# Kernel optimization log

Hardware: AMD Instinct MI355X
Metric: run time of the kernel (lower is better)

The kernel has to match this reference:

```python
import jax, jax.numpy as jnp
import numpy as np

L, S, R, NUM_RESNET = 6, 2, 3, 3
N = 2 ** L            # 64 blocks per axis
NX = N * S            # 128 grid points per axis
NCART_SIDE = 80
NCART = NCART_SIDE ** 2


def _perm_idx(L_, l):
    delta = 2 ** (L_ - l - 1)
    t = np.tile(np.arange(2) * delta, delta) + np.repeat(np.arange(delta), 2)
    t = np.tile(t, 2 ** l) + np.repeat(np.arange(2 ** l) * 2 ** (L_ - l), 2 ** (L_ - l))
    return jnp.asarray(t)


def _switch_idx(L_):
    h = L_ // 2
    t = np.tile(np.arange(2 ** h) * 2 ** h, 2 ** h) + np.repeat(np.arange(2 ** h), 2 ** h)
    return jnp.asarray(t)


def _bmm2(x, g_left, g_right):
    # x: (B,p,i,q,j). Right block-diag GEMM on (q,j), then left block-diag GEMM on (p,i).
    y = jnp.einsum('bpiqj,qjk->bpiqk', x, g_right)
    return jnp.einsum('bpiqk,pio->bpoqk', y, g_left)


def _complex_layer(xr, xi, p):
    # p: stacked (r1,i1,r2,i2,r3,i3,r4,i4); complex-style cross products of the original.
    r1, i1, r2, i2, r3, i3, r4, i4 = p
    yr = _bmm2(xr, r1, r1) + _bmm2(xr, i1, i1) + _bmm2(xi, r2, i2) + _bmm2(xi, i2, r2)
    yi = _bmm2(xi, r3, r3) + _bmm2(xi, i3, i3) + _bmm2(xr, r4, i4) + _bmm2(xr, i4, r4)
    return yr, yi


def _u_layer(xr, xi, p):
    ur1, ui1, ur2, ui2, ur3, ui3, ur4, ui4 = p
    return (_bmm2(xr, ur1, ur1) + _bmm2(xr, ui2, ui2)
            + _bmm2(xi, ur3, ui3) + _bmm2(xi, ui4, ur4))


def _permute(yr, yi, idx):
    yr = jnp.take(jnp.take(yr, idx, axis=1), idx, axis=3)
    yi = jnp.take(jnp.take(yi, idx, axis=1), idx, axis=3)
    return yr, yi


def _merge(y):  # (B,N,R,N,R) -> (B,N/2,2R,N/2,2R)
    return y.reshape(y.shape[0], N // 2, 2 * R, N // 2, 2 * R)


def _split(y):  # inverse of _merge
    return y.reshape(y.shape[0], N, R, N, R)


def reference(x, Vp, Hp, Mp, Gp, Up, cart_mat, r_index):
    B = x.shape[0]
    xr = x[..., 0].reshape(B, N, S, N, S)
    xi = x[..., 1].reshape(B, N, S, N, S)
    yr, yi = _complex_layer(xr, xi, Vp)                       # (B,N,R,N,R)
    for li, l in enumerate(range(L - 1, L // 2 - 1, -1)):     # H stages (permute then merge-GEMM)
        yr, yi = _permute(yr, yi, _perm_idx(L, l))
        yr, yi = _complex_layer(_merge(yr), _merge(yi), Hp[li])
        yr, yi = _split(yr), _split(yi)
    yr, yi = _permute(yr, yi, _switch_idx(L))                 # middle switch shuffle
    for k in range(NUM_RESNET):                               # residual M blocks
        zr, zi = _complex_layer(yr, yi, Mp[k])
        yr, yi = yr + zr, yi + zi
    for li, l in enumerate(range(L // 2 - 1, -1, -1)):        # G stages (merge-GEMM then permute)
        yr, yi = _complex_layer(_merge(yr), _merge(yi), Gp[li])
        yr, yi = _split(yr), _split(yi)
        yr, yi = _permute(yr, yi, _perm_idx(L, l))
    y = _u_layer(yr, yi, Up).reshape(B, NX * NX)              # real output, (B,NX,NX) flattened
    y = jnp.take(y, r_index, axis=1)                          # polar reindexing
    out = y @ cart_mat.T                                      # polar -> cartesian interpolation
    return out.reshape(B, NCART_SIDE, NCART_SIDE)


def setup_inputs() -> dict:
    key = jax.random.key(0)
    ks = jax.random.split(key, 9)
    B = 128
    x = jax.random.normal(ks[0], (B, NX, NX, 2), dtype=jnp.float32)
    Vp = jax.random.normal(ks[1], (8, N, S, R), dtype=jnp.float32) * 0.35
    Hp = jax.random.normal(ks[2], (L // 2, 8, N // 2, 2 * R, 2 * R), dtype=jnp.float32) * 0.2
    Mp = jax.random.normal(ks[3], (NUM_RESNET, 8, N, R, R), dtype=jnp.float32) * 0.25
    Gp = jax.random.normal(ks[4], (L // 2, 8, N // 2, 2 * R, 2 * R), dtype=jnp.float32) * 0.2
    Up = jax.random.normal(ks[5], (8, N, R, S), dtype=jnp.float32) * 0.35
    cart_mat = jax.random.normal(ks[6], (NCART, NX * NX), dtype=jnp.float32) * 0.01
    r_index = jax.random.permutation(ks[7], NX * NX).astype(jnp.int32)
    return {"x": x, "Vp": Vp, "Hp": Hp, "Mp": Mp, "Gp": Gp, "Up": Up,
            "cart_mat": cart_mat, "r_index": r_index}
```

## Files before the change

kernel.cpp:

```cpp
#include <hip/hip_runtime.h>


typedef __attribute__((ext_vector_type(8))) short sx8;
typedef __attribute__((ext_vector_type(4))) float fx4;
typedef __attribute__((ext_vector_type(8))) unsigned short usx8;
typedef __attribute__((ext_vector_type(4))) unsigned short usx4;

__device__ __forceinline__ unsigned short f2bf(float f) {
  unsigned u = __builtin_bit_cast(unsigned, f);
  u = (u + 0x7FFFu + ((u >> 16) & 1u)) >> 16;
  return (unsigned short)u;
}
__device__ __forceinline__ float bf2f(unsigned short h) {
  return __builtin_bit_cast(float, ((unsigned)h) << 16);
}

template<int ID>
__device__ __forceinline__ int rp_apply(int k) {
  if constexpr (ID == 0) { return k; }
  else if constexpr (ID == 3) { return (k & 7) * 8 + (k >> 3); }
  else {
    constexpr int l = (ID == 1) ? 4 : (ID == 2) ? 3 : (ID == 4) ? 2 : (ID == 5) ? 1 : 0;
    constexpr int d = 1 << (5 - l);
    constexpr int m2 = 2 * d;
    int g = k / m2, r = k % m2;
    return g * m2 + (r & 1) * d + (r >> 1);
  }
}

__global__ __launch_bounds__(256) void k_transpose(const float* __restrict__ x,
                                                   float* __restrict__ xtr,
                                                   float* __restrict__ xti) {
  __shared__ float ls[2][32][129];
  const int t = threadIdx.x;
  const int u = blockIdx.x;
  const int v0 = blockIdx.y * 32;
  for (int it = 0; it < 32; ++it) {
    int b = it * 4 + (t >> 6);
    int r = t & 63;
    int v = r >> 1, ch = r & 1;
    ls[ch][v][b] = x[(((size_t)b * 128 + u) * 128 + (v0 + v)) * 2 + ch];
  }
  __syncthreads();
  for (int it = 0; it < 32; ++it) {
    int idx = it * 256 + t;
    int ch = idx >> 12;
    int v = (idx >> 7) & 31;
    int b = idx & 127;
    float* dst = ch ? xti : xtr;
    dst[((size_t)(u * 128 + v0 + v)) * 128 + b] = ls[ch][v][b];
  }
}

__global__ __launch_bounds__(128) void k_vh(const float* __restrict__ xtr,
                                            const float* __restrict__ xti,
                                            float* __restrict__ yr,
                                            float* __restrict__ yi,
                                            const float* __restrict__ vp,
                                            const float* __restrict__ hp) {
  const int b = threadIdx.x;
  const int P = blockIdx.x, Q = blockIdx.y;
  float Vr[36], Vi[36];

#pragma unroll
  for (int pp = 0; pp < 2; ++pp)
#pragma unroll
    for (int qq = 0; qq < 2; ++qq) {
      const int p = 2 * P + pp, q = 2 * Q + qq;
      float Xr[4], Xi[4];
#pragma unroll
      for (int i = 0; i < 2; ++i)
#pragma unroll
        for (int j = 0; j < 2; ++j) {
          size_t off = ((size_t)((4 * P + 2 * pp + i) * 128 + (4 * Q + 2 * qq + j))) * 128 + b;
          Xr[i * 2 + j] = xtr[off];
          Xi[i * 2 + j] = xti[off];
        }
      float Ar[9], Ai[9];
#pragma unroll
      for (int k = 0; k < 9; ++k) { Ar[k] = 0.f; Ai[k] = 0.f; }
      auto termV = [&](float* Y, const float* X, int lm, int rm) {
        const float* Lw = vp + ((size_t)lm * 64 + p) * 6;
        const float* Rw = vp + ((size_t)rm * 64 + q) * 6;
#pragma unroll
        for (int i = 0; i < 2; ++i) {
          float t0 = X[i*2+0] * Rw[0] + X[i*2+1] * Rw[3];
          float t1 = X[i*2+0] * Rw[1] + X[i*2+1] * Rw[4];
          float t2 = X[i*2+0] * Rw[2] + X[i*2+1] * Rw[5];
#pragma unroll
          for (int o = 0; o < 3; ++o) {
            float lv = Lw[i * 3 + o];
            Y[o*3+0] += lv * t0; Y[o*3+1] += lv * t1; Y[o*3+2] += lv * t2;
          }
        }
      };
      termV(Ar, Xr, 0, 0); termV(Ar, Xr, 1, 1); termV(Ai, Xr, 6, 7); termV(Ai, Xr, 7, 6);
      termV(Ar, Xi, 2, 3); termV(Ar, Xi, 3, 2); termV(Ai, Xi, 4, 4); termV(Ai, Xi, 5, 5);
#pragma unroll
      for (int o = 0; o < 3; ++o)
#pragma unroll
        for (int k = 0; k < 3; ++k) {
          Vr[(3 * pp + o) * 6 + 3 * qq + k] = Ar[o * 3 + k];
          Vi[(3 * pp + o) * 6 + 3 * qq + k] = Ai[o * 3 + k];
        }
    }

  float Yr[36], Yi[36];
#pragma unroll
  for (int k = 0; k < 36; ++k) { Yr[k] = 0.f; Yi[k] = 0.f; }
  auto termH = [&](float* Y, const float* X, int lm, int rm) {
    const float* Lw = hp + ((size_t)lm * 32 + P) * 36;
    const float* Rw = hp + ((size_t)rm * 32 + Q) * 36;
#pragma unroll
    for (int i = 0; i < 6; ++i) {
      float tk[6];
#pragma unroll
      for (int k = 0; k < 6; ++k) tk[k] = 0.f;
#pragma unroll
      for (int j = 0; j < 6; ++j) {
        float xv = X[i * 6 + j];
#pragma unroll
        for (int k = 0; k < 6; ++k) tk[k] += xv * Rw[j * 6 + k];
      }
#pragma unroll
      for (int o = 0; o < 6; ++o) {
        float lv = Lw[i * 6 + o];
#pragma unroll
        for (int k = 0; k < 6; ++k) Y[o * 6 + k] += lv * tk[k];
      }
    }
  };
  termH(Yr, Vr, 0, 0); termH(Yr, Vr, 1, 1); termH(Yi, Vr, 6, 7); termH(Yi, Vr, 7, 6);
  termH(Yr, Vi, 2, 3); termH(Yr, Vi, 3, 2); termH(Yi, Vi, 4, 4); termH(Yi, Vi, 5, 5);

#pragma unroll
  for (int I = 0; I < 6; ++I)
#pragma unroll
    for (int J = 0; J < 6; ++J) {
      size_t off = ((size_t)((P * 6 + I) * 192 + (Q * 6 + J))) * 128 + b;
      yr[off] = Yr[I * 6 + J];
      yi[off] = Yi[I * 6 + J];
    }
}

template<int PERM>
__global__ __launch_bounds__(128) void k_hg(const float* __restrict__ xr,
                                            const float* __restrict__ xi,
                                            float* __restrict__ yr,
                                            float* __restrict__ yi,
                                            const float* __restrict__ wp) {
  const int b = threadIdx.x;
  const int P = blockIdx.x, Q = blockIdx.y;
  int rrow[6], rcol[6];
#pragma unroll
  for (int I = 0; I < 6; ++I) {
    rrow[I] = rp_apply<PERM>(2 * P + I / 3) * 3 + I % 3;
    rcol[I] = rp_apply<PERM>(2 * Q + I / 3) * 3 + I % 3;
  }
  float X[36], Yr[36], Yi[36];
#pragma unroll
  for (int k = 0; k < 36; ++k) { Yr[k] = 0.f; Yi[k] = 0.f; }

  auto loadX = [&](const float* src) {
#pragma unroll
    for (int I = 0; I < 6; ++I)
#pragma unroll
      for (int J = 0; J < 6; ++J)
        X[I * 6 + J] = src[((size_t)(rrow[I] * 192 + rcol[J])) * 128 + b];
  };
  auto term = [&](float* Y, int lm, int rm) {
    const float* Lw = wp + ((size_t)lm * 32 + P) * 36;
    const float* Rw = wp + ((size_t)rm * 32 + Q) * 36;
#pragma unroll
    for (int i = 0; i < 6; ++i) {
      float tk[6];
#pragma unroll
      for (int k = 0; k < 6; ++k) tk[k] = 0.f;
#pragma unroll
      for (int j = 0; j < 6; ++j) {
        float xv = X[i * 6 + j];
#pragma unroll
        for (int k = 0; k < 6; ++k) tk[k] += xv * Rw[j * 6 + k];
      }
#pragma unroll
      for (int o = 0; o < 6; ++o) {
        float lv = Lw[i * 6 + o];
#pragma unroll
        for (int k = 0; k < 6; ++k) Y[o * 6 + k] += lv * tk[k];
      }
    }
  };
  loadX(xr);
  term(Yr, 0, 0); term(Yr, 1, 1); term(Yi, 6, 7); term(Yi, 7, 6);
  loadX(xi);
  term(Yr, 2, 3); term(Yr, 3, 2); term(Yi, 4, 4); term(Yi, 5, 5);
#pragma unroll
  for (int I = 0; I < 6; ++I)
#pragma unroll
    for (int J = 0; J < 6; ++J) {
      size_t off = ((size_t)((P * 6 + I) * 192 + (Q * 6 + J))) * 128 + b;
      yr[off] = Yr[I * 6 + J];
      yi[off] = Yi[I * 6 + J];
    }
}

__global__ __launch_bounds__(128) void k_mg(const float* __restrict__ xr,
                                            const float* __restrict__ xi,
                                            float* __restrict__ yr,
                                            float* __restrict__ yi,
                                            const float* __restrict__ mp,
                                            const float* __restrict__ gp) {
  const int b = threadIdx.x;
  const int P = blockIdx.x, Q = blockIdx.y;
  float Vr[36], Vi[36];

#pragma unroll
  for (int aa = 0; aa < 2; ++aa)
#pragma unroll
    for (int bb = 0; bb < 2; ++bb) {
      const int p = 2 * P + aa, q = 2 * Q + bb;
      const int prow = rp_apply<3>(p) * 3, pcol = rp_apply<3>(q) * 3;
      float Xr[9], Xi[9];
#pragma unroll
      for (int i = 0; i < 3; ++i)
#pragma unroll
        for (int j = 0; j < 3; ++j) {
          size_t off = ((size_t)((prow + i) * 192 + (pcol + j))) * 128 + b;
          Xr[i * 3 + j] = xr[off];
          Xi[i * 3 + j] = xi[off];
        }
#pragma unroll
      for (int lk = 0; lk < 3; ++lk) {
        const float* wp = mp + (size_t)lk * (8 * 64 * 9);
        float Yr9[9], Yi9[9];
#pragma unroll
        for (int k = 0; k < 9; ++k) { Yr9[k] = Xr[k]; Yi9[k] = Xi[k]; }
        auto termM = [&](float* Y, const float* X, int lm, int rm) {
          const float* Lw = wp + ((size_t)lm * 64 + p) * 9;
          const float* Rw = wp + ((size_t)rm * 64 + q) * 9;
#pragma unroll
          for (int i = 0; i < 3; ++i) {
            float t0 = X[i*3+0] * Rw[0] + X[i*3+1] * Rw[3] + X[i*3+2] * Rw[6];
            float t1 = X[i*3+0] * Rw[1] + X[i*3+1] * Rw[4] + X[i*3+2] * Rw[7];
            float t2 = X[i*3+0] * Rw[2] + X[i*3+1] * Rw[5] + X[i*3+2] * Rw[8];
#pragma unroll
            for (int o = 0; o < 3; ++o) {
              float lv = Lw[i * 3 + o];
              Y[o*3+0] += lv * t0; Y[o*3+1] += lv * t1; Y[o*3+2] += lv * t2;
            }
          }
        };
        termM(Yr9, Xr, 0, 0); termM(Yr9, Xr, 1, 1); termM(Yi9, Xr, 6, 7); termM(Yi9, Xr, 7, 6);
        termM(Yr9, Xi, 2, 3); termM(Yr9, Xi, 3, 2); termM(Yi9, Xi, 4, 4); termM(Yi9, Xi, 5, 5);
#pragma unroll
        for (int k = 0; k < 9; ++k) { Xr[k] = Yr9[k]; Xi[k] = Yi9[k]; }
      }
#pragma unroll
      for (int i = 0; i < 3; ++i)
#pragma unroll
        for (int j = 0; j < 3; ++j) {
          Vr[(3 * aa + i) * 6 + 3 * bb + j] = Xr[i * 3 + j];
          Vi[(3 * aa + i) * 6 + 3 * bb + j] = Xi[i * 3 + j];
        }
    }

  float Yr[36], Yi[36];
#pragma unroll
  for (int k = 0; k < 36; ++k) { Yr[k] = 0.f; Yi[k] = 0.f; }
  auto termH = [&](float* Y, const float* X, int lm, int rm) {
    const float* Lw = gp + ((size_t)lm * 32 + P) * 36;
    const float* Rw = gp + ((size_t)rm * 32 + Q) * 36;
#pragma unroll
    for (int i = 0; i < 6; ++i) {
      float tk[6];
#pragma unroll
      for (int k = 0; k < 6; ++k) tk[k] = 0.f;
#pragma unroll
      for (int j = 0; j < 6; ++j) {
        float xv = X[i * 6 + j];
#pragma unroll
        for (int k = 0; k < 6; ++k) tk[k] += xv * Rw[j * 6 + k];
      }
#pragma unroll
      for (int o = 0; o < 6; ++o) {
        float lv = Lw[i * 6 + o];
#pragma unroll
        for (int k = 0; k < 6; ++k) Y[o * 6 + k] += lv * tk[k];
      }
    }
  };
  termH(Yr, Vr, 0, 0); termH(Yr, Vr, 1, 1); termH(Yi, Vr, 6, 7); termH(Yi, Vr, 7, 6);
  termH(Yr, Vi, 2, 3); termH(Yr, Vi, 3, 2); termH(Yi, Vi, 4, 4); termH(Yi, Vi, 5, 5);

#pragma unroll
  for (int I = 0; I < 6; ++I)
#pragma unroll
    for (int J = 0; J < 6; ++J) {
      size_t off = ((size_t)((P * 6 + I) * 192 + (Q * 6 + J))) * 128 + b;
      yr[off] = Yr[I * 6 + J];
      yi[off] = Yi[I * 6 + J];
    }
}

__global__ __launch_bounds__(128) void k_u(const float* __restrict__ xr,
                                           const float* __restrict__ xi,
                                           unsigned short* __restrict__ ut,
                                           const float* __restrict__ wp) {
  const int b = threadIdx.x;
  const int p = blockIdx.x, q = blockIdx.y;
  int rrow[3], rcol[3];
#pragma unroll
  for (int i = 0; i < 3; ++i) {
    rrow[i] = rp_apply<6>(p) * 3 + i;
    rcol[i] = rp_apply<6>(q) * 3 + i;
  }
  float X[9], Y[4] = {0.f, 0.f, 0.f, 0.f};
  auto loadX = [&](const float* src) {
#pragma unroll
    for (int i = 0; i < 3; ++i)
#pragma unroll
      for (int j = 0; j < 3; ++j)
        X[i * 3 + j] = src[((size_t)(rrow[i] * 192 + rcol[j])) * 128 + b];
  };
  auto term = [&](int lm, int rm) {
    const float* Lw = wp + ((size_t)lm * 64 + p) * 6;
    const float* Rw = wp + ((size_t)rm * 64 + q) * 6;
#pragma unroll
    for (int i = 0; i < 3; ++i) {
      float t0 = X[i*3+0] * Rw[0] + X[i*3+1] * Rw[2] + X[i*3+2] * Rw[4];
      float t1 = X[i*3+0] * Rw[1] + X[i*3+1] * Rw[3] + X[i*3+2] * Rw[5];
      Y[0] += Lw[i*2+0] * t0; Y[1] += Lw[i*2+0] * t1;
      Y[2] += Lw[i*2+1] * t0; Y[3] += Lw[i*2+1] * t1;
    }
  };
  loadX(xr); term(0, 0); term(3, 3);
  loadX(xi); term(4, 5); term(7, 6);
#pragma unroll
  for (int o = 0; o < 2; ++o)
#pragma unroll
    for (int k = 0; k < 2; ++k)
      ut[((size_t)((p * 2 + o) * 128 + (q * 2 + k))) * 128 + b] = f2bf(Y[o * 2 + k]);
}

__global__ __launch_bounds__(256) void k_gather(const unsigned short* __restrict__ ut,
                                                const int* __restrict__ r_index,
                                                unsigned short* __restrict__ yg) {
  __shared__ unsigned short ls[64][130];
  __shared__ int ridx[64];
  const int t = threadIdx.x;
  const int m0 = blockIdx.x * 64;
  if (t < 64) ridx[t] = r_index[m0 + t];
  __syncthreads();
  for (int it = 0; it < 32; ++it) {
    int idx = it * 256 + t;
    int ml = idx >> 7, b = idx & 127;
    ls[ml][b] = ut[(size_t)ridx[ml] * 128 + b];
  }
  __syncthreads();
  int b = t >> 1, half = t & 1;
#pragma unroll
  for (int c = 0; c < 4; ++c) {
    usx8 v;
#pragma unroll
    for (int e = 0; e < 8; ++e) v[e] = ls[half * 32 + c * 8 + e][b];
    *(usx8*)(yg + (size_t)b * 16384 + m0 + half * 32 + c * 8) = v;
  }
}

#define G2_KC 4
#define G2_STEPS 64
#define G2_PITCH 72

__global__ __launch_bounds__(256) void k_gemm2(const unsigned short* __restrict__ yg,
                                               const float* __restrict__ cart,
                                               float* __restrict__ partial) {
  __shared__ unsigned short As[2][128][G2_PITCH];
  __shared__ unsigned short Bs[2][64][G2_PITCH];
  const int t = threadIdx.x;
  const int lane = t & 63, w = t >> 6;
  const int kc = blockIdx.x;
  const int c0 = blockIdx.y * 64;
  const int k0 = kc * 4096;

  fx4 acc[2][4];
#pragma unroll
  for (int i = 0; i < 2; ++i)
#pragma unroll
    for (int j = 0; j < 4; ++j) acc[i][j] = (fx4)0.f;

  auto ldA = [&](int rep, int kpos) -> usx8 {
    int c = t + rep * 256;
    return *(const usx8*)(yg + (size_t)(c >> 3) * 16384 + kpos + (c & 7) * 8);
  };
  auto stA = [&](int buf, int rep, usx8 v) {
    int c = t + rep * 256;
    *(usx8*)(&As[buf][c >> 3][(c & 7) * 8]) = v;
  };
  auto ldB = [&](int rep, int kpos, fx4* f0, fx4* f1) {
    int c = t + rep * 256;
    const float* p = cart + (size_t)(c0 + (c >> 3)) * 16384 + kpos + (c & 7) * 8;
    *f0 = *(const fx4*)p;
    *f1 = *(const fx4*)(p + 4);
  };
  auto stB = [&](int buf, int rep, fx4 f0, fx4 f1) {
    int c = t + rep * 256;
    usx8 v;
    v[0]=f2bf(f0[0]); v[1]=f2bf(f0[1]); v[2]=f2bf(f0[2]); v[3]=f2bf(f0[3]);
    v[4]=f2bf(f1[0]); v[5]=f2bf(f1[1]); v[6]=f2bf(f1[2]); v[7]=f2bf(f1[3]);
    *(usx8*)(&Bs[buf][c >> 3][(c & 7) * 8]) = v;
  };

  {
    usx8 a0 = ldA(0, k0), a1 = ldA(1, k0), a2 = ldA(2, k0), a3 = ldA(3, k0);
    fx4 b00, b01, b10, b11;
    ldB(0, k0, &b00, &b01); ldB(1, k0, &b10, &b11);
    stA(0, 0, a0); stA(0, 1, a1); stA(0, 2, a2); stA(0, 3, a3);
    stB(0, 0, b00, b01); stB(0, 1, b10, b11);
  }
  __syncthreads();

  for (int s = 0; s < G2_STEPS; ++s) {
    const int cur = s & 1;
    usx8 av[4]; fx4 b00, b01, b10, b11;
    const bool pf = (s + 1 < G2_STEPS);
    if (pf) {
      int kpos = k0 + (s + 1) * 64;
      av[0] = ldA(0, kpos); av[1] = ldA(1, kpos);
      av[2] = ldA(2, kpos); av[3] = ldA(3, kpos);
      ldB(0, kpos, &b00, &b01); ldB(1, kpos, &b10, &b11);
    }
    sx8 af[2][2], bf[4][2];
#pragma unroll
    for (int mi = 0; mi < 2; ++mi)
#pragma unroll
      for (int kk = 0; kk < 2; ++kk)
        af[mi][kk] = *(const sx8*)(&As[cur][w * 32 + mi * 16 + (lane & 15)][kk * 32 + (lane >> 4) * 8]);
#pragma unroll
    for (int ni = 0; ni < 4; ++ni)
#pragma unroll
      for (int kk = 0; kk < 2; ++kk)
        bf[ni][kk] = *(const sx8*)(&Bs[cur][ni * 16 + (lane & 15)][kk * 32 + (lane >> 4) * 8]);
#pragma unroll
    for (int kk = 0; kk < 2; ++kk)
#pragma unroll
      for (int mi = 0; mi < 2; ++mi)
#pragma unroll
        for (int ni = 0; ni < 4; ++ni)
          acc[mi][ni] = __builtin_amdgcn_mfma_f32_16x16x32_bf16(af[mi][kk], bf[ni][kk], acc[mi][ni], 0, 0, 0);
    if (pf) {
      stA(cur ^ 1, 0, av[0]); stA(cur ^ 1, 1, av[1]);
      stA(cur ^ 1, 2, av[2]); stA(cur ^ 1, 3, av[3]);
      stB(cur ^ 1, 0, b00, b01); stB(cur ^ 1, 1, b10, b11);
    }
    __syncthreads();
  }

#pragma unroll
  for (int mi = 0; mi < 2; ++mi) {
    int brow = w * 32 + mi * 16 + (lane >> 4) * 4;
#pragma unroll
    for (int ni = 0; ni < 4; ++ni) {
      int cc = c0 + ni * 16 + (lane & 15);
#pragma unroll
      for (int r = 0; r < 4; ++r)
        partial[((size_t)kc * 128 + brow + r) * 6400 + cc] = acc[mi][ni][r];
    }
  }
}

__global__ __launch_bounds__(256) void k_reduce2(const float* __restrict__ partial,
                                                 float* __restrict__ out) {
  int i = blockIdx.x * 256 + threadIdx.x;
  fx4 s = (fx4)0.f;
#pragma unroll
  for (int kc = 0; kc < G2_KC; ++kc)
    s += *(const fx4*)(partial + (size_t)kc * 819200 + (size_t)i * 4);
  *(fx4*)(out + (size_t)i * 4) = s;
}

extern "C" void kernel_launch(void* const* d_in, const int* in_sizes, int n_in,
                              void* d_out, int out_size, void* d_ws, size_t ws_size,
                              hipStream_t stream) {
  const float* x    = (const float*)d_in[0];
  const float* Vp   = (const float*)d_in[1];
  const float* Hp   = (const float*)d_in[2];
  const float* Mp   = (const float*)d_in[3];
  const float* Gp   = (const float*)d_in[4];
  const float* Up   = (const float*)d_in[5];
  const float* cart = (const float*)d_in[6];
  const int*   ridx = (const int*)d_in[7];
  float* out = (float*)d_out;
  float* ws  = (float*)d_ws;

  const size_t PSZ = 4718592;
  float* P0r = ws;
  float* P0i = ws + PSZ;
  float* P1r = ws + 2 * PSZ;
  float* P1i = ws + 3 * PSZ;
  float* xtr = ws + 4 * PSZ;
  float* xti = xtr + 2097152;
  unsigned short* ut = (unsigned short*)(ws + 4 * PSZ);
  unsigned short* yg = (unsigned short*)(ws + 4 * PSZ + 1048576);
  float* partial = ws;

  const size_t HSZ = 8 * 32 * 36;

  k_transpose<<<dim3(128, 4), 256, 0, stream>>>(x, xtr, xti);
  k_vh<<<dim3(32, 32), 128, 0, stream>>>(xtr, xti, P0r, P0i, Vp, Hp + 0 * HSZ);
  k_hg<1><<<dim3(32, 32), 128, 0, stream>>>(P0r, P0i, P1r, P1i, Hp + 1 * HSZ);
  k_hg<2><<<dim3(32, 32), 128, 0, stream>>>(P1r, P1i, P0r, P0i, Hp + 2 * HSZ);
  k_mg<<<dim3(32, 32), 128, 0, stream>>>(P0r, P0i, P1r, P1i, Mp, Gp + 0 * HSZ);
  k_hg<4><<<dim3(32, 32), 128, 0, stream>>>(P1r, P1i, P0r, P0i, Gp + 1 * HSZ);
  k_hg<5><<<dim3(32, 32), 128, 0, stream>>>(P0r, P0i, P1r, P1i, Gp + 2 * HSZ);
  k_u<<<dim3(64, 64), 128, 0, stream>>>(P1r, P1i, ut, Up);
  k_gather<<<dim3(256), 256, 0, stream>>>(ut, ridx, yg);
  k_gemm2<<<dim3(G2_KC, 100), 256, 0, stream>>>(yg, cart, partial);
  k_reduce2<<<dim3(800), 256, 0, stream>>>(partial, out);
  (void)in_sizes; (void)n_in; (void)out_size; (void)ws_size;
}
```

Baseline: 342.4 us.

## Fuse butterfly stages into one cooperative persistent kernel with grid syncs

Merges the transpose, V/H, G, M, U and gather stages into a single cooperative kernel with a fixed grid of 512 blocks. Each stage loops over its work units, and stages are separated by grid.sync() instead of separate kernel launches. The aim is to remove launch overhead and inter-kernel gaps. In exchange, the grid is smaller than before (512 blocks of 128 threads versus 1024–4096 blocks), and __launch_bounds__(128,2) may constrain registers for the register-heavy stage bodies, which could cause spills or lower occupancy.

Measured after the change: 1.098 ms. 221% more time.

```diff
diff --git a/kernel.cpp b/kernel.cpp
--- a/kernel.cpp
+++ b/kernel.cpp
@@ -1,4 +1,7 @@
 #include <hip/hip_runtime.h>
+#include <hip/hip_cooperative_groups.h>
+
+namespace cg = cooperative_groups;
 
 
 typedef __attribute__((ext_vector_type(8))) short sx8;
@@ -10,9 +13,6 @@
   unsigned u = __builtin_bit_cast(unsigned, f);
   u = (u + 0x7FFFu + ((u >> 16) & 1u)) >> 16;
   return (unsigned short)u;
-}
-__device__ __forceinline__ float bf2f(unsigned short h) {
-  return __builtin_bit_cast(float, ((unsigned)h) << 16);
 }
 
 template<int ID>
@@ -28,40 +28,16 @@
   }
 }
 
-__global__ __launch_bounds__(256) void k_transpose(const float* __restrict__ x,
-                                                   float* __restrict__ xtr,
-                                                   float* __restrict__ xti) {
-  __shared__ float ls[2][32][129];
-  const int t = threadIdx.x;
-  const int u = blockIdx.x;
-  const int v0 = blockIdx.y * 32;
-  for (int it = 0; it < 32; ++it) {
-    int b = it * 4 + (t >> 6);
-    int r = t & 63;
-    int v = r >> 1, ch = r & 1;
-    ls[ch][v][b] = x[(((size_t)b * 128 + u) * 128 + (v0 + v)) * 2 + ch];
-  }
-  __syncthreads();
-  for (int it = 0; it < 32; ++it) {
-    int idx = it * 256 + t;
-    int ch = idx >> 12;
-    int v = (idx >> 7) & 31;
-    int b = idx & 127;
-    float* dst = ch ? xti : xtr;
-    dst[((size_t)(u * 128 + v0 + v)) * 128 + b] = ls[ch][v][b];
-  }
-}
-
-__global__ __launch_bounds__(128) void k_vh(const float* __restrict__ xtr,
-                                            const float* __restrict__ xti,
-                                            float* __restrict__ yr,
-                                            float* __restrict__ yi,
-                                            const float* __restrict__ vp,
-                                            const float* __restrict__ hp) {
-  const int b = threadIdx.x;
-  const int P = blockIdx.x, Q = blockIdx.y;
+
+__device__ __forceinline__ void vh_body(int unit, int b,
+                                        const float* __restrict__ xtr,
+                                        const float* __restrict__ xti,
+                                        float* __restrict__ yr,
+                                        float* __restrict__ yi,
+                                        const float* __restrict__ vp,
+                                        const float* __restrict__ hp) {
+  const int P = unit >> 5, Q = unit & 31;
   float Vr[36], Vi[36];
-
 #pragma unroll
   for (int pp = 0; pp < 2; ++pp)
 #pragma unroll
@@ -104,7 +80,6 @@
           Vi[(3 * pp + o) * 6 + 3 * qq + k] = Ai[o * 3 + k];
         }
     }
-
   float Yr[36], Yi[36];
 #pragma unroll
   for (int k = 0; k < 36; ++k) { Yr[k] = 0.f; Yi[k] = 0.f; }
@@ -132,7 +107,6 @@
   };
   termH(Yr, Vr, 0, 0); termH(Yr, Vr, 1, 1); termH(Yi, Vr, 6, 7); termH(Yi, Vr, 7, 6);
   termH(Yr, Vi, 2, 3); termH(Yr, Vi, 3, 2); termH(Yi, Vi, 4, 4); termH(Yi, Vi, 5, 5);
-
 #pragma unroll
   for (int I = 0; I < 6; ++I)
 #pragma unroll
@@ -144,13 +118,13 @@
 }
 
 template<int PERM>
-__global__ __launch_bounds__(128) void k_hg(const float* __restrict__ xr,
-                                            const float* __restrict__ xi,
-                                            float* __restrict__ yr,
-                                            float* __restrict__ yi,
-                                            const float* __restrict__ wp) {
-  const int b = threadIdx.x;
-  const int P = blockIdx.x, Q = blockIdx.y;
+__device__ __forceinline__ void hg_body(int unit, int b,
+                                        const float* __restrict__ xr,
+                                        const float* __restrict__ xi,
+                                        float* __restrict__ yr,
+                                        float* __restrict__ yi,
+                                        const float* __restrict__ wp) {
+  const int P = unit >> 5, Q = unit & 31;
   int rrow[6], rcol[6];
 #pragma unroll
   for (int I = 0; I < 6; ++I) {
@@ -160,7 +134,6 @@
   float X[36], Yr[36], Yi[36];
 #pragma unroll
   for (int k = 0; k < 36; ++k) { Yr[k] = 0.f; Yi[k] = 0.f; }
-
   auto loadX = [&](const float* src) {
 #pragma unroll
     for (int I = 0; I < 6; ++I)
@@ -204,16 +177,15 @@
     }
 }
 
-__global__ __launch_bounds__(128) void k_mg(const float* __restrict__ xr,
-                                            const float* __restrict__ xi,
-                                            float* __restrict__ yr,
-                                            float* __restrict__ yi,
-                                            const float* __restrict__ mp,
-                                            const float* __restrict__ gp) {
-  const int b = threadIdx.x;
-  const int P = blockIdx.x, Q = blockIdx.y;
+__device__ __forceinline__ void mg_body(int unit, int b,
+                                        const float* __restrict__ xr,
+                                        const float* __restrict__ xi,
+                                        float* __restrict__ yr,
+                                        float* __restrict__ yi,
+                                        const float* __restrict__ mp,
+                                        const float* __restrict__ gp) {
+  const int P = unit >> 5, Q = unit & 31;
   float Vr[36], Vi[36];
-
 #pragma unroll
   for (int aa = 0; aa < 2; ++aa)
 #pragma unroll
@@ -263,7 +235,6 @@
           Vi[(3 * aa + i) * 6 + 3 * bb + j] = Xi[i * 3 + j];
         }
     }
-
   float Yr[36], Yi[36];
 #pragma unroll
   for (int k = 0; k < 36; ++k) { Yr[k] = 0.f; Yi[k] = 0.f; }
@@ -291,7 +262,6 @@
   };
   termH(Yr, Vr, 0, 0); termH(Yr, Vr, 1, 1); termH(Yi, Vr, 6, 7); termH(Yi, Vr, 7, 6);
   termH(Yr, Vi, 2, 3); termH(Yr, Vi, 3, 2); termH(Yi, Vi, 4, 4); termH(Yi, Vi, 5, 5);
-
 #pragma unroll
   for (int I = 0; I < 6; ++I)
 #pragma unroll
@@ -302,12 +272,12 @@
     }
 }
 
-__global__ __launch_bounds__(128) void k_u(const float* __restrict__ xr,
-                                           const float* __restrict__ xi,
-                                           unsigned short* __restrict__ ut,
-                                           const float* __restrict__ wp) {
-  const int b = threadIdx.x;
-  const int p = blockIdx.x, q = blockIdx.y;
+__device__ __forceinline__ void u_body(int unit, int b,
+                                       const float* __restrict__ xr,
+                                       const float* __restrict__ xi,
+                                       unsigned short* __restrict__ ut,
+                                       const float* __restrict__ wp) {
+  const int p = unit >> 6, q = unit & 63;
   int rrow[3], rcol[3];
 #pragma unroll
   for (int i = 0; i < 3; ++i) {
@@ -342,28 +312,82 @@
       ut[((size_t)((p * 2 + o) * 128 + (q * 2 + k))) * 128 + b] = f2bf(Y[o * 2 + k]);
 }
 
-__global__ __launch_bounds__(256) void k_gather(const unsigned short* __restrict__ ut,
-                                                const int* __restrict__ r_index,
-                                                unsigned short* __restrict__ yg) {
-  __shared__ unsigned short ls[64][130];
-  __shared__ int ridx[64];
+#define MEGA_GRID 512
+
+__global__ __launch_bounds__(128, 2) void k_mega(
+    const float* __restrict__ x,
+    const float* __restrict__ vp, const float* __restrict__ hp,
+    const float* __restrict__ mp, const float* __restrict__ gp,
+    const float* __restrict__ up, const int* __restrict__ ridx,
+    float* p0r, float* p0i, float* p1r, float* p1i,
+    float* xtr, float* xti, unsigned short* ut, unsigned short* yg) {
+  cg::grid_group grid = cg::this_grid();
   const int t = threadIdx.x;
-  const int m0 = blockIdx.x * 64;
-  if (t < 64) ridx[t] = r_index[m0 + t];
-  __syncthreads();
-  for (int it = 0; it < 32; ++it) {
-    int idx = it * 256 + t;
-    int ml = idx >> 7, b = idx & 127;
-    ls[ml][b] = ut[(size_t)ridx[ml] * 128 + b];
-  }
-  __syncthreads();
-  int b = t >> 1, half = t & 1;
-#pragma unroll
-  for (int c = 0; c < 4; ++c) {
-    usx8 v;
-#pragma unroll
-    for (int e = 0; e < 8; ++e) v[e] = ls[half * 32 + c * 8 + e][b];
-    *(usx8*)(yg + (size_t)b * 16384 + m0 + half * 32 + c * 8) = v;
+  __shared__ __align__(16) unsigned char smem[16896];
+
+  {
+    float (*ls)[16][129] = (float (*)[16][129])smem;
+    for (int unit = blockIdx.x; unit < 1024; unit += MEGA_GRID) {
+      int u = unit >> 3, v0 = (unit & 7) * 16;
+      for (int it = 0; it < 32; ++it) {
+        int b = it * 4 + (t >> 5);
+        int r = t & 31;
+        int v = r >> 1, ch = r & 1;
+        ls[ch][v][b] = x[(((size_t)b * 128 + u) * 128 + (v0 + v)) * 2 + ch];
+      }
+      __syncthreads();
+      for (int it = 0; it < 32; ++it) {
+        int idx = it * 128 + t;
+        int b = idx & 127;
+        int v = (idx >> 7) & 15;
+        int ch = idx >> 11;
+        float* dst = ch ? xti : xtr;
+        dst[((size_t)(u * 128 + v0 + v)) * 128 + b] = ls[ch][v][b];
+      }
+      __syncthreads();
+    }
+  }
+  grid.sync();
+  for (int unit = blockIdx.x; unit < 1024; unit += MEGA_GRID)
+    vh_body(unit, t, xtr, xti, p0r, p0i, vp, hp + 0 * (8 * 32 * 36));
+  grid.sync();
+  for (int unit = blockIdx.x; unit < 1024; unit += MEGA_GRID)
+    hg_body<1>(unit, t, p0r, p0i, p1r, p1i, hp + 1 * (8 * 32 * 36));
+  grid.sync();
+  for (int unit = blockIdx.x; unit < 1024; unit += MEGA_GRID)
+    hg_body<2>(unit, t, p1r, p1i, p0r, p0i, hp + 2 * (8 * 32 * 36));
+  grid.sync();
+  for (int unit = blockIdx.x; unit < 1024; unit += MEGA_GRID)
+    mg_body(unit, t, p0r, p0i, p1r, p1i, mp, gp + 0 * (8 * 32 * 36));
+  grid.sync();
+  for (int unit = blockIdx.x; unit < 1024; unit += MEGA_GRID)
+    hg_body<4>(unit, t, p1r, p1i, p0r, p0i, gp + 1 * (8 * 32 * 36));
+  grid.sync();
+  for (int unit = blockIdx.x; unit < 1024; unit += MEGA_GRID)
+    hg_body<5>(unit, t, p0r, p0i, p1r, p1i, gp + 2 * (8 * 32 * 36));
+  grid.sync();
+  for (int unit = blockIdx.x; unit < 4096; unit += MEGA_GRID)
+    u_body(unit, t, p1r, p1i, ut, up);
+  grid.sync();
+  {
+    unsigned short (*ls)[130] = (unsigned short (*)[130])smem;
+    int* rl = (int*)(smem + 64 * 130 * 2);
+    for (int unit = blockIdx.x; unit < 256; unit += MEGA_GRID) {
+      int m0 = unit * 64;
+      if (t < 64) rl[t] = ridx[m0 + t];
+      __syncthreads();
+      for (int ml = 0; ml < 64; ++ml)
+        ls[ml][t] = ut[(size_t)rl[ml] * 128 + t];
+      __syncthreads();
+#pragma unroll
+      for (int c = 0; c < 8; ++c) {
+        usx8 v;
+#pragma unroll
+        for (int e = 0; e < 8; ++e) v[e] = ls[c * 8 + e][t];
+        *(usx8*)(yg + (size_t)t * 16384 + m0 + c * 8) = v;
+      }
+      __syncthreads();
+    }
   }
 }
 
@@ -503,17 +527,12 @@
   unsigned short* yg = (unsigned short*)(ws + 4 * PSZ + 1048576);
   float* partial = ws;
 
-  const size_t HSZ = 8 * 32 * 36;
-
-  k_transpose<<<dim3(128, 4), 256, 0, stream>>>(x, xtr, xti);
-  k_vh<<<dim3(32, 32), 128, 0, stream>>>(xtr, xti, P0r, P0i, Vp, Hp + 0 * HSZ);
-  k_hg<1><<<dim3(32, 32), 128, 0, stream>>>(P0r, P0i, P1r, P1i, Hp + 1 * HSZ);
-  k_hg<2><<<dim3(32, 32), 128, 0, stream>>>(P1r, P1i, P0r, P0i, Hp + 2 * HSZ);
-  k_mg<<<dim3(32, 32), 128, 0, stream>>>(P0r, P0i, P1r, P1i, Mp, Gp + 0 * HSZ);
-  k_hg<4><<<dim3(32, 32), 128, 0, stream>>>(P1r, P1i, P0r, P0i, Gp + 1 * HSZ);
-  k_hg<5><<<dim3(32, 32), 128, 0, stream>>>(P0r, P0i, P1r, P1i, Gp + 2 * HSZ);
-  k_u<<<dim3(64, 64), 128, 0, stream>>>(P1r, P1i, ut, Up);
-  k_gather<<<dim3(256), 256, 0, stream>>>(ut, ridx, yg);
+  void* args[] = {(void*)&x, (void*)&Vp, (void*)&Hp, (void*)&Mp, (void*)&Gp,
+                  (void*)&Up, (void*)&ridx,
+                  (void*)&P0r, (void*)&P0i, (void*)&P1r, (void*)&P1i,
+                  (void*)&xtr, (void*)&xti, (void*)&ut, (void*)&yg};
+  hipLaunchCooperativeKernel((void*)k_mega, dim3(MEGA_GRID), dim3(128),
+                             args, 0, stream);
   k_gemm2<<<dim3(G2_KC, 100), 256, 0, stream>>>(yg, cart, partial);
   k_reduce2<<<dim3(800), 256, 0, stream>>>(partial, out);
   (void)in_sizes; (void)n_in; (void)out_size; (void)ws_size;
```

## Store butterfly intermediates in fp16 and bf16 split-K partials with more K chunks

Applied to the files above, without the earlier changes.

Switches every intermediate activation buffer between the butterfly stages (transpose output, P0/P1 ping-pong) from fp32 to fp16 storage, with all compute still in fp32 registers. The final GEMM's split-K partials are now written as bf16, and the split-K factor doubles to 8 chunks of 2048. The goal is to halve the memory traffic of these bandwidth-bound per-batch stages and to give the GEMM more blocks. The trade-off is lower precision in the intermediates and partial sums, including possible fp16 range or rounding problems and larger error from bf16 partials.

New measurement: 333.2 us. 2.7% less time.

```diff
diff --git a/kernel.cpp b/kernel.cpp
--- a/kernel.cpp
+++ b/kernel.cpp
@@ -1,6 +1,7 @@
 #include <hip/hip_runtime.h>
 
 
+typedef _Float16 f16;
 typedef __attribute__((ext_vector_type(8))) short sx8;
 typedef __attribute__((ext_vector_type(4))) float fx4;
 typedef __attribute__((ext_vector_type(8))) unsigned short usx8;
@@ -29,8 +30,8 @@
 }
 
 __global__ __launch_bounds__(256) void k_transpose(const float* __restrict__ x,
-                                                   float* __restrict__ xtr,
-                                                   float* __restrict__ xti) {
+                                                   f16* __restrict__ xtr,
+                                                   f16* __restrict__ xti) {
   __shared__ float ls[2][32][129];
   const int t = threadIdx.x;
   const int u = blockIdx.x;
@@ -47,15 +48,15 @@
     int ch = idx >> 12;
     int v = (idx >> 7) & 31;
     int b = idx & 127;
-    float* dst = ch ? xti : xtr;
-    dst[((size_t)(u * 128 + v0 + v)) * 128 + b] = ls[ch][v][b];
-  }
-}
-
-__global__ __launch_bounds__(128) void k_vh(const float* __restrict__ xtr,
-                                            const float* __restrict__ xti,
-                                            float* __restrict__ yr,
-                                            float* __restrict__ yi,
+    f16* dst = ch ? xti : xtr;
+    dst[((size_t)(u * 128 + v0 + v)) * 128 + b] = (f16)ls[ch][v][b];
+  }
+}
+
+__global__ __launch_bounds__(128) void k_vh(const f16* __restrict__ xtr,
+                                            const f16* __restrict__ xti,
+                                            f16* __restrict__ yr,
+                                            f16* __restrict__ yi,
                                             const float* __restrict__ vp,
                                             const float* __restrict__ hp) {
   const int b = threadIdx.x;
@@ -73,8 +74,8 @@
 #pragma unroll
         for (int j = 0; j < 2; ++j) {
           size_t off = ((size_t)((4 * P + 2 * pp + i) * 128 + (4 * Q + 2 * qq + j))) * 128 + b;
-          Xr[i * 2 + j] = xtr[off];
-          Xi[i * 2 + j] = xti[off];
+          Xr[i * 2 + j] = (float)xtr[off];
+          Xi[i * 2 + j] = (float)xti[off];
         }
       float Ar[9], Ai[9];
 #pragma unroll
@@ -138,16 +139,16 @@
 #pragma unroll
     for (int J = 0; J < 6; ++J) {
       size_t off = ((size_t)((P * 6 + I) * 192 + (Q * 6 + J))) * 128 + b;
-      yr[off] = Yr[I * 6 + J];
-      yi[off] = Yi[I * 6 + J];
+      yr[off] = (f16)Yr[I * 6 + J];
+      yi[off] = (f16)Yi[I * 6 + J];
     }
 }
 
 template<int PERM>
-__global__ __launch_bounds__(128) void k_hg(const float* __restrict__ xr,
-                                            const float* __restrict__ xi,
-                                            float* __restrict__ yr,
-                                            float* __restrict__ yi,
+__global__ __launch_bounds__(128) void k_hg(const f16* __restrict__ xr,
+                                            const f16* __restrict__ xi,
+                                            f16* __restrict__ yr,
+                                            f16* __restrict__ yi,
                                             const float* __restrict__ wp) {
   const int b = threadIdx.x;
   const int P = blockIdx.x, Q = blockIdx.y;
@@ -161,12 +162,12 @@
 #pragma unroll
   for (int k = 0; k < 36; ++k) { Yr[k] = 0.f; Yi[k] = 0.f; }
 
-  auto loadX = [&](const float* src) {
+  auto loadX = [&](const f16* src) {
 #pragma unroll
     for (int I = 0; I < 6; ++I)
 #pragma unroll
       for (int J = 0; J < 6; ++J)
-        X[I * 6 + J] = src[((size_t)(rrow[I] * 192 + rcol[J])) * 128 + b];
+        X[I * 6 + J] = (float)src[((size_t)(rrow[I] * 192 + rcol[J])) * 128 + b];
   };
   auto term = [&](float* Y, int lm, int rm) {
     const float* Lw = wp + ((size_t)lm * 32 + P) * 36;
@@ -199,15 +200,15 @@
 #pragma unroll
     for (int J = 0; J < 6; ++J) {
       size_t off = ((size_t)((P * 6 + I) * 192 + (Q * 6 + J))) * 128 + b;
-      yr[off] = Yr[I * 6 + J];
-      yi[off] = Yi[I * 6 + J];
-    }
-}
-
-__global__ __launch_bounds__(128) void k_mg(const float* __restrict__ xr,
-                                            const float* __restrict__ xi,
-                                            float* __restrict__ yr,
-                                            float* __restrict__ yi,
+      yr[off] = (f16)Yr[I * 6 + J];
+      yi[off] = (f16)Yi[I * 6 + J];
+    }
+}
+
+__global__ __launch_bounds__(128) void k_mg(const f16* __restrict__ xr,
+                                            const f16* __restrict__ xi,
+                                            f16* __restrict__ yr,
+                                            f16* __restrict__ yi,
                                             const float* __restrict__ mp,
                                             const float* __restrict__ gp) {
   const int b = threadIdx.x;
@@ -226,8 +227,8 @@
 #pragma unroll
         for (int j = 0; j < 3; ++j) {
           size_t off = ((size_t)((prow + i) * 192 + (pcol + j))) * 128 + b;
-          Xr[i * 3 + j] = xr[off];
-          Xi[i * 3 + j] = xi[off];
+          Xr[i * 3 + j] = (float)xr[off];
+          Xi[i * 3 + j] = (float)xi[off];
         }
 #pragma unroll
       for (int lk = 0; lk < 3; ++lk) {
@@ -297,13 +298,13 @@
 #pragma unroll
     for (int J = 0; J < 6; ++J) {
       size_t off = ((size_t)((P * 6 + I) * 192 + (Q * 6 + J))) * 128 + b;
-      yr[off] = Yr[I * 6 + J];
-      yi[off] = Yi[I * 6 + J];
-    }
-}
-
-__global__ __launch_bounds__(128) void k_u(const float* __restrict__ xr,
-                                           const float* __restrict__ xi,
+      yr[off] = (f16)Yr[I * 6 + J];
+      yi[off] = (f16)Yi[I * 6 + J];
+    }
+}
+
+__global__ __launch_bounds__(128) void k_u(const f16* __restrict__ xr,
+                                           const f16* __restrict__ xi,
                                            unsigned short* __restrict__ ut,
                                            const float* __restrict__ wp) {
   const int b = threadIdx.x;
@@ -315,12 +316,12 @@
     rcol[i] = rp_apply<6>(q) * 3 + i;
   }
   float X[9], Y[4] = {0.f, 0.f, 0.f, 0.f};
-  auto loadX = [&](const float* src) {
+  auto loadX = [&](const f16* src) {
 #pragma unroll
     for (int i = 0; i < 3; ++i)
 #pragma unroll
       for (int j = 0; j < 3; ++j)
-        X[i * 3 + j] = src[((size_t)(rrow[i] * 192 + rcol[j])) * 128 + b];
+        X[i * 3 + j] = (float)src[((size_t)(rrow[i] * 192 + rcol[j])) * 128 + b];
   };
   auto term = [&](int lm, int rm) {
     const float* Lw = wp + ((size_t)lm * 64 + p) * 6;
@@ -367,20 +368,20 @@
   }
 }
 
-#define G2_KC 4
-#define G2_STEPS 64
+#define G2_KC 8
+#define G2_STEPS 32
 #define G2_PITCH 72
 
 __global__ __launch_bounds__(256) void k_gemm2(const unsigned short* __restrict__ yg,
                                                const float* __restrict__ cart,
-                                               float* __restrict__ partial) {
+                                               unsigned short* __restrict__ partial) {
   __shared__ unsigned short As[2][128][G2_PITCH];
   __shared__ unsigned short Bs[2][64][G2_PITCH];
   const int t = threadIdx.x;
   const int lane = t & 63, w = t >> 6;
   const int kc = blockIdx.x;
   const int c0 = blockIdx.y * 64;
-  const int k0 = kc * 4096;
+  const int k0 = kc * 2048;
 
   fx4 acc[2][4];
 #pragma unroll
@@ -463,18 +464,20 @@
       int cc = c0 + ni * 16 + (lane & 15);
 #pragma unroll
       for (int r = 0; r < 4; ++r)
-        partial[((size_t)kc * 128 + brow + r) * 6400 + cc] = acc[mi][ni][r];
-    }
-  }
-}
-
-__global__ __launch_bounds__(256) void k_reduce2(const float* __restrict__ partial,
+        partial[((size_t)kc * 128 + brow + r) * 6400 + cc] = f2bf(acc[mi][ni][r]);
+    }
+  }
+}
+
+__global__ __launch_bounds__(256) void k_reduce2(const unsigned short* __restrict__ partial,
                                                  float* __restrict__ out) {
   int i = blockIdx.x * 256 + threadIdx.x;
   fx4 s = (fx4)0.f;
 #pragma unroll
-  for (int kc = 0; kc < G2_KC; ++kc)
-    s += *(const fx4*)(partial + (size_t)kc * 819200 + (size_t)i * 4);
+  for (int kc = 0; kc < G2_KC; ++kc) {
+    usx4 v = *(const usx4*)(partial + (size_t)kc * 819200 + (size_t)i * 4);
+    s[0] += bf2f(v[0]); s[1] += bf2f(v[1]); s[2] += bf2f(v[2]); s[3] += bf2f(v[3]);
+  }
   *(fx4*)(out + (size_t)i * 4) = s;
 }
 
@@ -490,18 +493,18 @@
   const float* cart = (const float*)d_in[6];
   const int*   ridx = (const int*)d_in[7];
   float* out = (float*)d_out;
-  float* ws  = (float*)d_ws;
+  unsigned short* hb = (unsigned short*)d_ws;
 
   const size_t PSZ = 4718592;
-  float* P0r = ws;
-  float* P0i = ws + PSZ;
-  float* P1r = ws + 2 * PSZ;
-  float* P1i = ws + 3 * PSZ;
-  float* xtr = ws + 4 * PSZ;
-  float* xti = xtr + 2097152;
-  unsigned short* ut = (unsigned short*)(ws + 4 * PSZ);
-  unsigned short* yg = (unsigned short*)(ws + 4 * PSZ + 1048576);
-  float* partial = ws;
+  f16* P0r = (f16*)(hb);
+  f16* P0i = (f16*)(hb + PSZ);
+  f16* P1r = (f16*)(hb + 2 * PSZ);
+  f16* P1i = (f16*)(hb + 3 * PSZ);
+  f16* xtr = (f16*)(hb + 4 * PSZ);
+  f16* xti = (f16*)(hb + 4 * PSZ + 2097152);
+  unsigned short* ut = hb + 4 * PSZ;
+  unsigned short* yg = hb + 4 * PSZ + 2097152;
+  unsigned short* partial = hb;
 
   const size_t HSZ = 8 * 32 * 36;
 
```
